# Kernel tuning notes

Measured on AMD Instinct MI355X. Metric: run time of the kernel, lower is better.

## Reference

```python
import jax, jax.numpy as jnp
import numpy as np

FEATURES = 768

def setup_inputs() -> dict:
    key = jax.random.key(0)
    k1, k2, kq, kd, kc = jax.random.split(key, 5)
    B, S1, S2 = 8, 2048, 2048
    bound = 1.0 / np.sqrt(FEATURES)  # nn.Linear default init range
    return {
        "matrix1": jax.random.normal(k1, (B, S1, FEATURES), dtype=jnp.float32),
        "matrix2": jax.random.normal(k2, (B, S2, FEATURES), dtype=jnp.float32),
        "w_q": jax.random.uniform(kq, (FEATURES,), jnp.float32, -bound, bound),
        "w_d": jax.random.uniform(kd, (FEATURES,), jnp.float32, -bound, bound),
        "w_c": jax.random.uniform(kc, (FEATURES,), jnp.float32, -bound, bound),
    }

def reference(matrix1, matrix2, w_q, w_d, w_c):
    # S[b,j,k] = (m1 @ w_q)[b,j] + (m2 @ w_d)[b,k] + sum_f w_c[f]*m1[b,j,f]*m2[b,k,f]
    Q = jnp.einsum('bjf,f->bj', matrix1, w_q)                # [B, S1]
    D = jnp.einsum('bkf,f->bk', matrix2, w_d)                # [B, S2]
    C = jnp.einsum('bjf,bkf->bjk', matrix1 * w_c, matrix2)   # [B, S1, S2]
    return Q[:, :, None] + D[:, None, :] + C
```

## Files before the change

### kernel.cpp

```cpp
#include <hip/hip_runtime.h>
#include <hip/hip_bf16.h>

#define S1 2048
#define S2 2048
#define FEAT 768
#define NB 8
#define BM 128
#define BN 128
#define BK 64
#define KSTEPS (FEAT / BK)

typedef __attribute__((ext_vector_type(8))) short bf16x8;
typedef __attribute__((ext_vector_type(4))) float f32x4;
typedef __attribute__((ext_vector_type(4))) unsigned short us4;
typedef __attribute__((address_space(1))) const unsigned int gu32;
typedef __attribute__((address_space(3))) unsigned int lu32;

static __device__ __forceinline__ unsigned short f2bf(float x) {
    unsigned u = __builtin_bit_cast(unsigned, x);
    unsigned r = u + 0x7FFFu + ((u >> 16) & 1u);
    return (unsigned short)(r >> 16);
}

__global__ __launch_bounds__(256) void conv_kernel(
    const float* __restrict__ m1, const float* __restrict__ m2,
    const float* __restrict__ wq, const float* __restrict__ wd,
    const float* __restrict__ wc,
    unsigned short* __restrict__ A, unsigned short* __restrict__ Bm,
    float* __restrict__ Q, float* __restrict__ D) {
    int wave = threadIdx.x >> 6;
    int lane = threadIdx.x & 63;
    int g = blockIdx.x * 4 + wave;
    bool isA = (g < NB * S1);
    int row = isA ? g : g - NB * S1;
    const float* src = isA ? m1 : m2;
    const float* w   = isA ? wq : wd;
    unsigned short* dst = (isA ? A : Bm) + (size_t)row * FEAT;
    const float4* rp = (const float4*)(src + (size_t)row * FEAT);
    const float4* wp = (const float4*)w;
    const float4* cp = (const float4*)wc;
    float acc = 0.f;
#pragma unroll
    for (int i = 0; i < 3; ++i) {
        int idx = lane + 64 * i;
        float4 a = rp[idx];
        float4 b = wp[idx];
        acc += a.x * b.x + a.y * b.y + a.z * b.z + a.w * b.w;
        float4 c;
        if (isA) c = cp[idx]; else c = float4{1.f, 1.f, 1.f, 1.f};
        us4 v = { f2bf(a.x * c.x), f2bf(a.y * c.y),
                  f2bf(a.z * c.z), f2bf(a.w * c.w) };
        *(us4*)(dst + idx * 4) = v;
    }
#pragma unroll
    for (int s = 32; s; s >>= 1) acc += __shfl_xor(acc, s, 64);
    if (lane == 0) (isA ? Q : D)[row] = acc;
}

__global__ __launch_bounds__(256) void gemm_bf16_kernel(
    const unsigned short* __restrict__ A, const unsigned short* __restrict__ Bm,
    const float* __restrict__ Q, const float* __restrict__ D,
    float* __restrict__ out) {

    __shared__ __align__(16) char sA[BM * BK * 2];
    __shared__ __align__(16) char sB[BN * BK * 2];

    const int bid = blockIdx.x;
    const int swz = (bid & 7) * (NB * 256 / 8) + (bid >> 3);
    const int b  = swz >> 8;
    const int t  = swz & 255;
    const int tm = t >> 4, tn = t & 15;

    const int tid = threadIdx.x;
    const int lane = tid & 63;
    const int wave = tid >> 6;
    const int wm = wave >> 1, wn = wave & 1;

    const char* Ab = (const char*)(A + ((size_t)b * S1 + (size_t)tm * BM) * FEAT);
    const char* Bb = (const char*)(Bm + ((size_t)b * S2 + (size_t)tn * BN) * FEAT);

    const int srow = lane >> 3;
    const int scb  = 16 * ((lane & 7) ^ srow);

    f32x4 acc[4][4];
#pragma unroll
    for (int m = 0; m < 4; ++m)
#pragma unroll
        for (int n = 0; n < 4; ++n) acc[m][n] = (f32x4)0.f;

    for (int ks = 0; ks < KSTEPS; ++ks) {
        __syncthreads();
        const char* Aks = Ab + (size_t)ks * (BK * 2);
        const char* Bks = Bb + (size_t)ks * (BK * 2);
#pragma unroll
        for (int c = 0; c < 4; ++c) {
            int chunk = c * 4 + wave;
            int r = chunk * 8 + srow;
            __builtin_amdgcn_global_load_lds(
                (gu32*)(Aks + (size_t)r * (FEAT * 2) + scb),
                (lu32*)(sA + chunk * 1024), 16, 0, 0);
        }
#pragma unroll
        for (int c = 0; c < 4; ++c) {
            int chunk = c * 4 + wave;
            int r = chunk * 8 + srow;
            __builtin_amdgcn_global_load_lds(
                (gu32*)(Bks + (size_t)r * (FEAT * 2) + scb),
                (lu32*)(sB + chunk * 1024), 16, 0, 0);
        }
        __syncthreads();

#pragma unroll
        for (int s = 0; s < 2; ++s) {
            bf16x8 af[4], bfr[4];
#pragma unroll
            for (int m = 0; m < 4; ++m) {
                int r = wm * 64 + m * 16 + (lane & 15);
                int coff = (s * 64 + ((lane >> 4) * 16)) ^ ((r & 7) << 4);
                af[m] = *(const bf16x8*)(sA + r * 128 + coff);
            }
#pragma unroll
            for (int n = 0; n < 4; ++n) {
                int r = wn * 64 + n * 16 + (lane & 15);
                int coff = (s * 64 + ((lane >> 4) * 16)) ^ ((r & 7) << 4);
                bfr[n] = *(const bf16x8*)(sB + r * 128 + coff);
            }
#pragma unroll
            for (int m = 0; m < 4; ++m)
#pragma unroll
                for (int n = 0; n < 4; ++n)
                    acc[m][n] = __builtin_amdgcn_mfma_f32_16x16x32_bf16(
                        af[m], bfr[n], acc[m][n], 0, 0, 0);
        }
    }

    const float* Qb = Q + b * S1 + tm * BM;
    const float* Db = D + b * S2 + tn * BN;
    float dv[4];
#pragma unroll
    for (int n = 0; n < 4; ++n) dv[n] = Db[wn * 64 + n * 16 + (lane & 15)];

    const size_t outbase = ((size_t)b * S1 + (size_t)tm * BM) * S2 + (size_t)tn * BN;
#pragma unroll
    for (int m = 0; m < 4; ++m) {
#pragma unroll
        for (int i = 0; i < 4; ++i) {
            int rl = wm * 64 + m * 16 + (lane >> 4) * 4 + i;
            float qv = Qb[rl];
            float* orow = out + outbase + (size_t)rl * S2 + wn * 64;
#pragma unroll
            for (int n = 0; n < 4; ++n) {
                int cl = n * 16 + (lane & 15);
                orow[cl] = acc[m][n][i] + qv + dv[n];
            }
        }
    }
}

__global__ __launch_bounds__(256) void qd_kernel(
    const float* __restrict__ m1, const float* __restrict__ m2,
    const float* __restrict__ wq, const float* __restrict__ wd,
    float* __restrict__ Q, float* __restrict__ D) {
    int wave = threadIdx.x >> 6;
    int lane = threadIdx.x & 63;
    int g = blockIdx.x * 4 + wave;
    const float* src; const float* w; float* dst; int row;
    if (g < NB * S1) { src = m1; w = wq; dst = Q; row = g; }
    else             { src = m2; w = wd; dst = D; row = g - NB * S1; }
    const float4* rp = (const float4*)(src + (size_t)row * FEAT);
    const float4* wp = (const float4*)w;
    float acc = 0.f;
#pragma unroll
    for (int i = 0; i < 3; ++i) {
        float4 a = rp[lane + 64 * i];
        float4 b = wp[lane + 64 * i];
        acc += a.x * b.x + a.y * b.y + a.z * b.z + a.w * b.w;
    }
#pragma unroll
    for (int s = 32; s; s >>= 1) acc += __shfl_xor(acc, s, 64);
    if (lane == 0) dst[row] = acc;
}

__global__ __launch_bounds__(256) void gemm_kernel(
    const float* __restrict__ m1, const float* __restrict__ m2,
    const float* __restrict__ wc,
    const float* __restrict__ Q, const float* __restrict__ D,
    float* __restrict__ out) {

    __shared__ __align__(16) char sA[BM * BK * 2];
    __shared__ __align__(16) char sB[BN * BK * 2];
    __shared__ float wcs[FEAT];

    const int tid = threadIdx.x;
    const int blk = blockIdx.x;
    const int b  = blk >> 8;
    const int t  = blk & 255;
    const int tm = t >> 4, tn = t & 15;

    for (int i = tid; i < FEAT; i += 256) wcs[i] = wc[i];

    const float* Abase = m1 + ((size_t)b * S1 + (size_t)tm * BM) * FEAT;
    const float* Bbase = m2 + ((size_t)b * S2 + (size_t)tn * BN) * FEAT;

    const int lane = tid & 63;
    const int wave = tid >> 6;
    const int wm = wave >> 1, wn = wave & 1;

    f32x4 acc[4][4];
#pragma unroll
    for (int m = 0; m < 4; ++m)
#pragma unroll
        for (int n = 0; n < 4; ++n) acc[m][n] = (f32x4)0.f;

    const int col4 = tid & 15;
    const int row0 = tid >> 4;

    __syncthreads();

    for (int ks = 0; ks < FEAT / BK; ++ks) {
        float4 wc4 = *(const float4*)&wcs[ks * BK + col4 * 4];
        const float4* Ak = (const float4*)(Abase + ks * BK);
        const float4* Bk = (const float4*)(Bbase + ks * BK);

        __syncthreads();
#pragma unroll
        for (int i = 0; i < 8; ++i) {
            int r = row0 + 16 * i;
            float4 a = Ak[(size_t)r * (FEAT / 4) + col4];
            us4 av = { f2bf(a.x * wc4.x), f2bf(a.y * wc4.y),
                       f2bf(a.z * wc4.z), f2bf(a.w * wc4.w) };
            int off = r * 128 + ((col4 * 8) ^ ((r & 7) << 4));
            *(us4*)(sA + off) = av;
        }
#pragma unroll
        for (int i = 0; i < 8; ++i) {
            int r = row0 + 16 * i;
            float4 v = Bk[(size_t)r * (FEAT / 4) + col4];
            us4 bv = { f2bf(v.x), f2bf(v.y), f2bf(v.z), f2bf(v.w) };
            int off = r * 128 + ((col4 * 8) ^ ((r & 7) << 4));
            *(us4*)(sB + off) = bv;
        }
        __syncthreads();

#pragma unroll
        for (int s = 0; s < 2; ++s) {
            bf16x8 af[4], bfr[4];
#pragma unroll
            for (int m = 0; m < 4; ++m) {
                int r = wm * 64 + m * 16 + (lane & 15);
                int coff = (s * 64 + (lane >> 4) * 16) ^ ((r & 7) << 4);
                af[m] = *(const bf16x8*)(sA + r * 128 + coff);
            }
#pragma unroll
            for (int n = 0; n < 4; ++n) {
                int r = wn * 64 + n * 16 + (lane & 15);
                int coff = (s * 64 + (lane >> 4) * 16) ^ ((r & 7) << 4);
                bfr[n] = *(const bf16x8*)(sB + r * 128 + coff);
            }
#pragma unroll
            for (int m = 0; m < 4; ++m)
#pragma unroll
                for (int n = 0; n < 4; ++n)
                    acc[m][n] = __builtin_amdgcn_mfma_f32_16x16x32_bf16(
                        af[m], bfr[n], acc[m][n], 0, 0, 0);
        }
    }

    const float* Qb = Q + b * S1 + tm * BM;
    const float* Db = D + b * S2 + tn * BN;
    float dv[4];
#pragma unroll
    for (int n = 0; n < 4; ++n) dv[n] = Db[wn * 64 + n * 16 + (lane & 15)];

    const size_t outbase = ((size_t)b * S1 + (size_t)tm * BM) * S2 + (size_t)tn * BN;
#pragma unroll
    for (int m = 0; m < 4; ++m) {
#pragma unroll
        for (int i = 0; i < 4; ++i) {
            int rl = wm * 64 + m * 16 + (lane >> 4) * 4 + i;
            float qv = Qb[rl];
            float* orow = out + outbase + (size_t)rl * S2 + wn * 64;
#pragma unroll
            for (int n = 0; n < 4; ++n) {
                int cl = n * 16 + (lane & 15);
                orow[cl] = acc[m][n][i] + qv + dv[n];
            }
        }
    }
}

extern "C" void kernel_launch(void* const* d_in, const int* in_sizes, int n_in,
                              void* d_out, int out_size, void* d_ws, size_t ws_size,
                              hipStream_t stream) {
    const float* m1 = (const float*)d_in[0];
    const float* m2 = (const float*)d_in[1];
    const float* wq = (const float*)d_in[2];
    const float* wd = (const float*)d_in[3];
    const float* wc = (const float*)d_in[4];
    float* out = (float*)d_out;

    const size_t elems = (size_t)NB * S1 * FEAT;
    const size_t need = 2 * elems * sizeof(unsigned short)
                      + (size_t)(NB * S1 + NB * S2) * sizeof(float);

    if (ws_size >= need) {
        unsigned short* Abuf = (unsigned short*)d_ws;
        unsigned short* Bbuf = Abuf + elems;
        float* Q  = (float*)(Bbuf + elems);
        float* Dv = Q + NB * S1;
        conv_kernel<<<(NB * S1 + NB * S2) / 4, 256, 0, stream>>>(
            m1, m2, wq, wd, wc, Abuf, Bbuf, Q, Dv);
        gemm_bf16_kernel<<<NB * 256, 256, 0, stream>>>(Abuf, Bbuf, Q, Dv, out);
    } else {
        float* Q  = (float*)d_ws;
        float* Dv = Q + NB * S1;
        qd_kernel<<<(2 * NB * S1) / 4, 256, 0, stream>>>(m1, m2, wq, wd, Q, Dv);
        gemm_kernel<<<NB * 256, 256, 0, stream>>>(m1, m2, wc, Q, Dv, out);
    }
}
```

Before: 101.0 us.

## Replace bf16 GEMM with 256x256-tile multi-buffered pipelined kernel

```diff
diff --git a/kernel.cpp b/kernel.cpp
--- a/kernel.cpp
+++ b/kernel.cpp
@@ -5,10 +5,12 @@
 #define S2 2048
 #define FEAT 768
 #define NB 8
-#define BM 128
-#define BN 128
-#define BK 64
-#define KSTEPS (FEAT / BK)
+#define BM 256
+#define BN 256
+#define BK 32
+#define NKT (FEAT / BK)
+#define KTILE_BYTES 32768
+#define NBUF 4
 
 typedef __attribute__((ext_vector_type(8))) short bf16x8;
 typedef __attribute__((ext_vector_type(4))) float f32x4;
@@ -57,80 +59,92 @@
     if (lane == 0) (isA ? Q : D)[row] = acc;
 }
 
-__global__ __launch_bounds__(256) void gemm_bf16_kernel(
+#define STAGE(kt) do {                                                            \
+    const int _buf = (kt) & (NBUF - 1);                                           \
+    const char* _As = Ab + (kt) * (BK * 2);                                       \
+    const char* _Bs = Bb + (kt) * (BK * 2);                                       \
+    char* _lA = ldsb + _buf * KTILE_BYTES;                                        \
+    char* _lB = _lA + 16384;                                                      \
+    _Pragma("unroll")                                                             \
+    for (int _r = 0; _r < 2; ++_r) {                                              \
+        const int _rowb = _r * 128 + wave * 16;                                   \
+        __builtin_amdgcn_global_load_lds(                                         \
+            (gu32*)(_As + (size_t)(_rowb + srow) * (FEAT * 2) + scol),            \
+            (lu32*)(_lA + _rowb * 64), 16, 0, 0);                                 \
+        __builtin_amdgcn_global_load_lds(                                         \
+            (gu32*)(_Bs + (size_t)(_rowb + srow) * (FEAT * 2) + scol),            \
+            (lu32*)(_lB + _rowb * 64), 16, 0, 0);                                 \
+    }                                                                             \
+} while (0)
+
+__global__ __launch_bounds__(512, 2) void gemm256_kernel(
     const unsigned short* __restrict__ A, const unsigned short* __restrict__ Bm,
     const float* __restrict__ Q, const float* __restrict__ D,
     float* __restrict__ out) {
 
-    __shared__ __align__(16) char sA[BM * BK * 2];
-    __shared__ __align__(16) char sB[BN * BK * 2];
+    extern __shared__ __align__(16) char ldsb[];
 
     const int bid = blockIdx.x;
-    const int swz = (bid & 7) * (NB * 256 / 8) + (bid >> 3);
-    const int b  = swz >> 8;
-    const int t  = swz & 255;
-    const int tm = t >> 4, tn = t & 15;
-
-    const int tid = threadIdx.x;
+    const int swz = (bid & 7) * 64 + (bid >> 3);
+    const int b  = swz >> 6;
+    const int t  = swz & 63;
+    const int tm = t >> 3, tn = t & 7;
+
+    const int tid  = threadIdx.x;
     const int lane = tid & 63;
     const int wave = tid >> 6;
-    const int wm = wave >> 1, wn = wave & 1;
+    const int wm = wave >> 2, wn = wave & 3;
 
     const char* Ab = (const char*)(A + ((size_t)b * S1 + (size_t)tm * BM) * FEAT);
     const char* Bb = (const char*)(Bm + ((size_t)b * S2 + (size_t)tn * BN) * FEAT);
 
-    const int srow = lane >> 3;
-    const int scb  = 16 * ((lane & 7) ^ srow);
-
-    f32x4 acc[4][4];
-#pragma unroll
-    for (int m = 0; m < 4; ++m)
+    const int srow = lane >> 2;
+    const int scol = (lane & 3) * 16;
+
+    const int fr   = lane & 15;
+    const int fkg  = (lane >> 4) * 16;
+
+    f32x4 acc[8][4];
+#pragma unroll
+    for (int m = 0; m < 8; ++m)
 #pragma unroll
         for (int n = 0; n < 4; ++n) acc[m][n] = (f32x4)0.f;
 
-    for (int ks = 0; ks < KSTEPS; ++ks) {
-        __syncthreads();
-        const char* Aks = Ab + (size_t)ks * (BK * 2);
-        const char* Bks = Bb + (size_t)ks * (BK * 2);
-#pragma unroll
-        for (int c = 0; c < 4; ++c) {
-            int chunk = c * 4 + wave;
-            int r = chunk * 8 + srow;
-            __builtin_amdgcn_global_load_lds(
-                (gu32*)(Aks + (size_t)r * (FEAT * 2) + scb),
-                (lu32*)(sA + chunk * 1024), 16, 0, 0);
-        }
-#pragma unroll
-        for (int c = 0; c < 4; ++c) {
-            int chunk = c * 4 + wave;
-            int r = chunk * 8 + srow;
-            __builtin_amdgcn_global_load_lds(
-                (gu32*)(Bks + (size_t)r * (FEAT * 2) + scb),
-                (lu32*)(sB + chunk * 1024), 16, 0, 0);
-        }
-        __syncthreads();
-
-#pragma unroll
-        for (int s = 0; s < 2; ++s) {
-            bf16x8 af[4], bfr[4];
-#pragma unroll
-            for (int m = 0; m < 4; ++m) {
-                int r = wm * 64 + m * 16 + (lane & 15);
-                int coff = (s * 64 + ((lane >> 4) * 16)) ^ ((r & 7) << 4);
-                af[m] = *(const bf16x8*)(sA + r * 128 + coff);
-            }
-#pragma unroll
-            for (int n = 0; n < 4; ++n) {
-                int r = wn * 64 + n * 16 + (lane & 15);
-                int coff = (s * 64 + ((lane >> 4) * 16)) ^ ((r & 7) << 4);
-                bfr[n] = *(const bf16x8*)(sB + r * 128 + coff);
-            }
-#pragma unroll
-            for (int m = 0; m < 4; ++m)
-#pragma unroll
-                for (int n = 0; n < 4; ++n)
-                    acc[m][n] = __builtin_amdgcn_mfma_f32_16x16x32_bf16(
-                        af[m], bfr[n], acc[m][n], 0, 0, 0);
+    STAGE(0);
+    STAGE(1);
+    asm volatile("s_waitcnt vmcnt(4)" ::: "memory");
+    __builtin_amdgcn_s_barrier();
+    asm volatile("" ::: "memory");
+
+#pragma unroll 4
+    for (int kt = 0; kt < NKT; ++kt) {
+        if (kt + 2 < NKT) STAGE(kt + 2);
+
+        const char* lA = ldsb + (kt & (NBUF - 1)) * KTILE_BYTES;
+        const char* lB = lA + 16384;
+
+        bf16x8 bfr[4], af[8];
+#pragma unroll
+        for (int n = 0; n < 4; ++n)
+            bfr[n] = *(const bf16x8*)(lB + (wn * 64 + n * 16 + fr) * 64 + fkg);
+#pragma unroll
+        for (int m = 0; m < 8; ++m)
+            af[m] = *(const bf16x8*)(lA + (wm * 128 + m * 16 + fr) * 64 + fkg);
+
+        __builtin_amdgcn_s_setprio(1);
+#pragma unroll
+        for (int m = 0; m < 8; ++m)
+#pragma unroll
+            for (int n = 0; n < 4; ++n)
+                acc[m][n] = __builtin_amdgcn_mfma_f32_16x16x32_bf16(
+                    af[m], bfr[n], acc[m][n], 0, 0, 0);
+        __builtin_amdgcn_s_setprio(0);
+
+        if (kt + 1 < NKT) {
+            if (kt + 2 < NKT) asm volatile("s_waitcnt vmcnt(4)" ::: "memory");
+            else              asm volatile("s_waitcnt vmcnt(0)" ::: "memory");
+            __builtin_amdgcn_s_barrier();
+            asm volatile("" ::: "memory");
         }
     }
 
@@ -138,21 +152,19 @@
     const float* Db = D + b * S2 + tn * BN;
     float dv[4];
 #pragma unroll
-    for (int n = 0; n < 4; ++n) dv[n] = Db[wn * 64 + n * 16 + (lane & 15)];
+    for (int n = 0; n < 4; ++n) dv[n] = Db[wn * 64 + n * 16 + fr];
 
     const size_t outbase = ((size_t)b * S1 + (size_t)tm * BM) * S2 + (size_t)tn * BN;
 #pragma unroll
-    for (int m = 0; m < 4; ++m) {
+    for (int m = 0; m < 8; ++m) {
 #pragma unroll
         for (int i = 0; i < 4; ++i) {
-            int rl = wm * 64 + m * 16 + (lane >> 4) * 4 + i;
+            int rl = wm * 128 + m * 16 + (lane >> 4) * 4 + i;
             float qv = Qb[rl];
             float* orow = out + outbase + (size_t)rl * S2 + wn * 64;
 #pragma unroll
-            for (int n = 0; n < 4; ++n) {
-                int cl = n * 16 + (lane & 15);
-                orow[cl] = acc[m][n][i] + qv + dv[n];
-            }
+            for (int n = 0; n < 4; ++n)
+                orow[n * 16 + fr] = acc[m][n][i] + qv + dv[n];
         }
     }
 }
@@ -187,8 +199,8 @@
     const float* __restrict__ Q, const float* __restrict__ D,
     float* __restrict__ out) {
 
-    __shared__ __align__(16) char sA[BM * BK * 2];
-    __shared__ __align__(16) char sB[BN * BK * 2];
+    __shared__ __align__(16) char sA[128 * 64 * 2];
+    __shared__ __align__(16) char sB[128 * 64 * 2];
     __shared__ float wcs[FEAT];
 
     const int tid = threadIdx.x;
@@ -199,8 +211,8 @@
 
     for (int i = tid; i < FEAT; i += 256) wcs[i] = wc[i];
 
-    const float* Abase = m1 + ((size_t)b * S1 + (size_t)tm * BM) * FEAT;
-    const float* Bbase = m2 + ((size_t)b * S2 + (size_t)tn * BN) * FEAT;
+    const float* Abase = m1 + ((size_t)b * S1 + (size_t)tm * 128) * FEAT;
+    const float* Bbase = m2 + ((size_t)b * S2 + (size_t)tn * 128) * FEAT;
 
     const int lane = tid & 63;
     const int wave = tid >> 6;
@@ -217,10 +229,10 @@
 
     __syncthreads();
 
-    for (int ks = 0; ks < FEAT / BK; ++ks) {
-        float4 wc4 = *(const float4*)&wcs[ks * BK + col4 * 4];
-        const float4* Ak = (const float4*)(Abase + ks * BK);
-        const float4* Bk = (const float4*)(Bbase + ks * BK);
+    for (int ks = 0; ks < FEAT / 64; ++ks) {
+        float4 wc4 = *(const float4*)&wcs[ks * 64 + col4 * 4];
+        const float4* Ak = (const float4*)(Abase + ks * 64);
+        const float4* Bk = (const float4*)(Bbase + ks * 64);
 
         __syncthreads();
 #pragma unroll
@@ -266,13 +278,13 @@
         }
     }
 
-    const float* Qb = Q + b * S1 + tm * BM;
-    const float* Db = D + b * S2 + tn * BN;
+    const float* Qb = Q + b * S1 + tm * 128;
+    const float* Db = D + b * S2 + tn * 128;
     float dv[4];
 #pragma unroll
     for (int n = 0; n < 4; ++n) dv[n] = Db[wn * 64 + n * 16 + (lane & 15)];
 
-    const size_t outbase = ((size_t)b * S1 + (size_t)tm * BM) * S2 + (size_t)tn * BN;
+    const size_t outbase = ((size_t)b * S1 + (size_t)tm * 128) * S2 + (size_t)tn * 128;
 #pragma unroll
     for (int m = 0; m < 4; ++m) {
 #pragma unroll
@@ -310,7 +322,8 @@
         float* Dv = Q + NB * S1;
         conv_kernel<<<(NB * S1 + NB * S2) / 4, 256, 0, stream>>>(
             m1, m2, wq, wd, wc, Abuf, Bbuf, Q, Dv);
-        gemm_bf16_kernel<<<NB * 256, 256, 0, stream>>>(Abuf, Bbuf, Q, Dv, out);
+        gemm256_kernel<<<NB * (S1 / BM) * (S2 / BN), 512, NBUF * KTILE_BYTES, stream>>>(
+            Abuf, Bbuf, Q, Dv, out);
     } else {
         float* Q  = (float*)d_ws;
         float* Dv = Q + NB * S1;
```

Result: faster. 95.30 us (-5.6%).
